# Kernel optimization log

Hardware: AMD Instinct MI355X
Metric: run time of the kernel (lower is better)

## Reference

```python
import jax, jax.numpy as jnp
import numpy as np

NUM_GRAPHS = 256
BN_EPS = 1e-5
GN_EPS = 1e-5


def setup_inputs() -> dict:
    key = jax.random.key(0)
    ks = jax.random.split(key, 8)
    N, E, D, H = 100000, 600000, 128, 128
    x = jax.random.normal(ks[0], (N, D), dtype=jnp.float32)
    W1 = jax.random.normal(ks[1], (4, 4 * H, D), dtype=jnp.float32) * 0.05
    bn_g = jnp.ones((4, 4 * H), dtype=jnp.float32)
    bn_b = jnp.zeros((4, 4 * H), dtype=jnp.float32)
    W2 = jax.random.normal(ks[2], (4, H, 4 * H), dtype=jnp.float32) * 0.05
    b2 = jnp.zeros((4, H), dtype=jnp.float32)
    gn_g = jnp.ones((4, H), dtype=jnp.float32)
    gn_b = jnp.zeros((4, H), dtype=jnp.float32)
    gn_a = jnp.ones((4, H), dtype=jnp.float32)
    edge_index = jax.random.randint(ks[3], (2, E), 0, N, dtype=jnp.int64)
    batch = jnp.sort(jax.random.randint(ks[4], (N,), 0, NUM_GRAPHS, dtype=jnp.int64))
    return {"x": x, "W1": W1, "bn_g": bn_g, "bn_b": bn_b, "W2": W2, "b2": b2,
            "gn_g": gn_g, "gn_b": gn_b, "gn_a": gn_a,
            "edge_index": edge_index, "batch": batch}


def reference(x, W1, bn_g, bn_b, W2, b2, gn_g, gn_b, gn_a, edge_index, batch):
    N = x.shape[0]
    src, dst = edge_index[0], edge_index[1]
    # per-graph node counts (shared by GraphNorm and mean-pool)
    cnt = jax.ops.segment_sum(jnp.ones((N,), x.dtype), batch, num_segments=NUM_GRAPHS)
    cnt = jnp.maximum(cnt, 1.0)[:, None]  # [G,1]

    h = x
    hs = []
    for l in range(4):  # fixed small layer loop
        # GINConv: (1+eps)*x + sum_{j->i} x_j, eps=0 default
        agg = jax.ops.segment_sum(h[src], dst, num_segments=N)
        z = h + agg
        # MLP: Linear(no bias) -> BatchNorm1d (batch stats) -> SELU -> Linear
        z = z @ W1[l].T
        mu = jnp.mean(z, axis=0)
        var = jnp.mean((z - mu) ** 2, axis=0)
        z = (z - mu) * jax.lax.rsqrt(var + BN_EPS) * bn_g[l] + bn_b[l]
        z = jax.nn.selu(z)
        z = z @ W2[l].T + b2[l]
        # GraphNorm: per-graph mean/var with learnable mean scale alpha
        gmean = jax.ops.segment_sum(z, batch, num_segments=NUM_GRAPHS) / cnt
        sub = z - gn_a[l] * gmean[batch]
        gvar = jax.ops.segment_sum(sub * sub, batch, num_segments=NUM_GRAPHS) / cnt
        z = gn_g[l] * sub * jax.lax.rsqrt(gvar[batch] + GN_EPS) + gn_b[l]
        z = jax.nn.selu(z)  # self.act (SELU, matching MLP)
        hs.append(z)
        h = z

    hg = jnp.concatenate(hs, axis=1)  # [N, 4*H]
    pooled = jax.ops.segment_sum(hg, batch, num_segments=NUM_GRAPHS) / cnt
    return pooled
```

## Files before the change

### kernel.cpp

```cpp
#include <hip/hip_runtime.h>
#include <hip/hip_bf16.h>


typedef __attribute__((ext_vector_type(8))) short bf16x8;
typedef __attribute__((ext_vector_type(4))) float f32x4;

__device__ __forceinline__ unsigned short f2b(float x){
    __hip_bfloat16 h = __float2bfloat16(x);
    return *reinterpret_cast<unsigned short*>(&h);
}
__device__ __forceinline__ float b2f(unsigned short u){
    __hip_bfloat16 h;
    *reinterpret_cast<unsigned short*>(&h) = u;
    return __bfloat162float(h);
}
__device__ __forceinline__ float selu_f(float x){
    const float sc = 1.0507009873554805f, al = 1.6732632423543772f;
    return x > 0.f ? sc * x : sc * al * (__expf(x) - 1.f);
}

__global__ void count_kernel(const int* __restrict__ dst, int* __restrict__ counts, int E){
    int e = blockIdx.x * 256 + threadIdx.x;
    if (e < E) atomicAdd(&counts[dst[e]], 1);
}

__global__ void cnt_bs_kernel(const int* __restrict__ batch, float* __restrict__ cnt, int N){
    __shared__ int sb[257];
    int g = threadIdx.x;
    int lo = 0, hi = N;
    while (lo < hi){ int mid = (lo + hi) >> 1; if (batch[mid] < g) lo = mid + 1; else hi = mid; }
    sb[g] = lo;
    if (g == 0) sb[256] = N;
    __syncthreads();
    cnt[g] = fmaxf((float)(sb[g + 1] - sb[g]), 1.f);
}

__global__ __launch_bounds__(1024) void scan_kernel(const int* __restrict__ counts,
                                                    int* __restrict__ row_ptr, int N){
    __shared__ int wsum[16];
    __shared__ int wpre[16];
    __shared__ int s_total;
    __shared__ int s_running;
    int tid = threadIdx.x;
    int lane = tid & 63, wid = tid >> 6;
    if (tid == 0) s_running = 0;
    __syncthreads();
    for (int base = 0; base < N; base += 4096){
        int idx0 = base + tid * 4;
        int v[4];
        #pragma unroll
        for (int j = 0; j < 4; j++) v[j] = (idx0 + j < N) ? counts[idx0 + j] : 0;
        int tsum = v[0] + v[1] + v[2] + v[3];
        int x = tsum;
        #pragma unroll
        for (int off = 1; off < 64; off <<= 1){
            int y = __shfl_up(x, off, 64);
            if (lane >= off) x += y;
        }
        if (lane == 63) wsum[wid] = x;
        __syncthreads();
        if (wid == 0 && lane < 16){
            int w = wsum[lane];
            int xx = w;
            #pragma unroll
            for (int off = 1; off < 16; off <<= 1){
                int y = __shfl_up(xx, off, 64);
                if (lane >= off) xx += y;
            }
            wpre[lane] = xx - w;
            if (lane == 15) s_total = xx;
        }
        __syncthreads();
        int run = s_running + wpre[wid] + (x - tsum);
        #pragma unroll
        for (int j = 0; j < 4; j++){
            if (idx0 + j < N) row_ptr[idx0 + j] = run;
            run += v[j];
        }
        __syncthreads();
        if (tid == 0) s_running += s_total;
        __syncthreads();
    }
    if (tid == 0) row_ptr[N] = s_running;
}

__global__ void fill_kernel(const int* __restrict__ ei, const int* __restrict__ row_ptr,
                            int* __restrict__ fill, int* __restrict__ colv, int E){
    int e = blockIdx.x * 256 + threadIdx.x;
    if (e < E){
        int s = ei[e];
        int d = ei[E + e];
        int pos = atomicAdd(&fill[d], 1);
        colv[row_ptr[d] + pos] = s;
    }
}

__global__ void pack_kernel(const float* __restrict__ W1, const float* __restrict__ W2,
                            unsigned short* __restrict__ W1p, unsigned short* __restrict__ W2p){
    int t = blockIdx.x * 256 + threadIdx.x;
    int which = t >> 15;
    int u = t & 32767;
    int lane = u & 63; u >>= 6;
    int nf = u & 3; u >>= 2;
    int wc = u & 1; u >>= 1;
    int kk = u & 3; u >>= 2;
    int c = u & 3; u >>= 2;
    int l = u;
    int col = wc * 64 + nf * 16 + (lane & 15);
    int kbase = kk * 32 + (lane >> 4) * 8;
    size_t ob = ((((((size_t)(l * 4 + c) * 4 + kk) * 2 + wc) * 4 + nf) * 2) * 512) + lane * 8;
    unsigned short* dst = which == 0 ? W1p : W2p;
    #pragma unroll
    for (int j = 0; j < 8; j++){
        int k = kbase + j;
        float wv = which == 0 ? W1[((size_t)(l * 512) + c * 128 + col) * 128 + k]
                              : W2[((size_t)(l * 128) + col) * 512 + c * 128 + k];
        unsigned short hi = f2b(wv);
        unsigned short lo = f2b(wv - b2f(hi));
        dst[ob + j] = hi;
        dst[ob + 512 + j] = lo;
    }
}

__global__ __launch_bounds__(256) void agg_split_kernel(
    const float* __restrict__ h, const int* __restrict__ row_ptr,
    const int* __restrict__ colv,
    unsigned short* __restrict__ zhi, unsigned short* __restrict__ zlo, int N)
{
    int t = blockIdx.x * 256 + threadIdx.x;
    int i = t >> 5;
    if (i >= N) return;
    int vo = (t & 31);
    const float4* hv = reinterpret_cast<const float4*>(h);
    int p0 = row_ptr[i], p1 = row_ptr[i + 1];
    float4 acc = hv[(size_t)i * 32 + vo];
    int p = p0;
    for (; p + 4 <= p1; p += 4){
        int s0 = colv[p], s1 = colv[p + 1], s2 = colv[p + 2], s3 = colv[p + 3];
        float4 a = hv[(size_t)s0 * 32 + vo];
        float4 b = hv[(size_t)s1 * 32 + vo];
        float4 c = hv[(size_t)s2 * 32 + vo];
        float4 d = hv[(size_t)s3 * 32 + vo];
        acc.x += (a.x + b.x) + (c.x + d.x);
        acc.y += (a.y + b.y) + (c.y + d.y);
        acc.z += (a.z + b.z) + (c.z + d.z);
        acc.w += (a.w + b.w) + (c.w + d.w);
    }
    for (; p < p1; p++){
        float4 a = hv[(size_t)colv[p] * 32 + vo];
        acc.x += a.x; acc.y += a.y; acc.z += a.z; acc.w += a.w;
    }
    float vals[4] = {acc.x, acc.y, acc.z, acc.w};
    unsigned int h01, h23, l01, l23;
    {
        unsigned short hh[4], ll[4];
        #pragma unroll
        for (int j = 0; j < 4; j++){
            hh[j] = f2b(vals[j]);
            ll[j] = f2b(vals[j] - b2f(hh[j]));
        }
        h01 = (unsigned int)hh[0] | ((unsigned int)hh[1] << 16);
        h23 = (unsigned int)hh[2] | ((unsigned int)hh[3] << 16);
        l01 = (unsigned int)ll[0] | ((unsigned int)ll[1] << 16);
        l23 = (unsigned int)ll[2] | ((unsigned int)ll[3] << 16);
    }
    int kk = vo >> 3, kg = (vo >> 1) & 3, half = vo & 1;
    size_t fo = ((size_t)(i >> 4) * 4 + kk) * 512 + (kg * 16 + (i & 15)) * 8 + half * 4;
    *reinterpret_cast<uint2*>(zhi + fo) = make_uint2(h01, h23);
    *reinterpret_cast<uint2*>(zlo + fo) = make_uint2(l01, l23);
}

__global__ __launch_bounds__(512) void stats_k(
    const unsigned short* __restrict__ Zhi_g, const unsigned short* __restrict__ Zlo_g,
    const unsigned short* __restrict__ Bp, float* __restrict__ bn_acc, int N)
{
    __shared__ __align__(16) unsigned short Zh_s[16384];
    __shared__ __align__(16) unsigned short Zl_s[16384];
    int tid = threadIdx.x, lane = tid & 63, w = tid >> 6;
    int wr = w >> 2, wq = w & 3;
    int r_lo = lane & 15, kg = lane >> 4;
    int m0 = blockIdx.x * 128;

    {
        size_t gbase = (size_t)(m0 >> 4) * 2048;
        const uint4* gh = reinterpret_cast<const uint4*>(Zhi_g + gbase);
        const uint4* gl = reinterpret_cast<const uint4*>(Zlo_g + gbase);
        uint4* sh4 = reinterpret_cast<uint4*>(Zh_s);
        uint4* sl4 = reinterpret_cast<uint4*>(Zl_s);
        #pragma unroll
        for (int j = 0; j < 4; j++){
            sh4[j * 512 + tid] = gh[j * 512 + tid];
            sl4[j * 512 + tid] = gl[j * 512 + tid];
        }
    }
    __syncthreads();

    int wc = wq >> 1;
    for (int c = 0; c < 4; c++){
        const bf16x8* Bv = reinterpret_cast<const bf16x8*>(Bp) + (size_t)c * 4096;
        f32x4 acc[4][2];
        #pragma unroll
        for (int i = 0; i < 4; i++)
            #pragma unroll
            for (int j = 0; j < 2; j++) acc[i][j] = (f32x4){0.f, 0.f, 0.f, 0.f};

        for (int kk = 0; kk < 4; kk++){
            bf16x8 bh[2], bl[2];
            #pragma unroll
            for (int nf = 0; nf < 2; nf++){
                int nfold = (wq & 1) * 2 + nf;
                int ob = ((kk * 2 + wc) * 4 + nfold) * 2;
                bh[nf] = Bv[(ob + 0) * 64 + lane];
                bl[nf] = Bv[(ob + 1) * 64 + lane];
            }
            bf16x8 ah[4], alr[4];
            #pragma unroll
            for (int mf = 0; mf < 4; mf++){
                int so = ((wr * 4 + mf) * 4 + kk) * 512 + lane * 8;
                ah[mf]  = *reinterpret_cast<const bf16x8*>(&Zh_s[so]);
                alr[mf] = *reinterpret_cast<const bf16x8*>(&Zl_s[so]);
            }
            #pragma unroll
            for (int mf = 0; mf < 4; mf++)
                #pragma unroll
                for (int nf = 0; nf < 2; nf++){
                    acc[mf][nf] = __builtin_amdgcn_mfma_f32_16x16x32_bf16(ah[mf],  bh[nf], acc[mf][nf], 0, 0, 0);
                    acc[mf][nf] = __builtin_amdgcn_mfma_f32_16x16x32_bf16(ah[mf],  bl[nf], acc[mf][nf], 0, 0, 0);
                    acc[mf][nf] = __builtin_amdgcn_mfma_f32_16x16x32_bf16(alr[mf], bh[nf], acc[mf][nf], 0, 0, 0);
                }
        }

        #pragma unroll
        for (int nf = 0; nf < 2; nf++){
            int col = wq * 32 + nf * 16 + r_lo;
            float s = 0.f, q = 0.f;
            #pragma unroll
            for (int mf = 0; mf < 4; mf++)
                #pragma unroll
                for (int r = 0; r < 4; r++){
                    int row = m0 + wr * 64 + mf * 16 + kg * 4 + r;
                    if (row < N){
                        float v = acc[mf][nf][r];
                        s += v; q += v * v;
                    }
                }
            s += __shfl_xor(s, 16); s += __shfl_xor(s, 32);
            q += __shfl_xor(q, 16); q += __shfl_xor(q, 32);
            if (lane < 16){
                atomicAdd(&bn_acc[c * 256 + col], s);
                atomicAdd(&bn_acc[c * 256 + 128 + col], q);
            }
        }
    }
}

__global__ void bn_final_k(const float* __restrict__ bn_acc,
                           const float* __restrict__ bng, const float* __restrict__ bnb,
                           float* __restrict__ sc, float* __restrict__ sh,
                           int l, float invN){
    int colg = threadIdx.x;
    float s = bn_acc[(colg >> 7) * 256 + (colg & 127)];
    float q = bn_acc[(colg >> 7) * 256 + 128 + (colg & 127)];
    float mu = s * invN;
    float var = q * invN - mu * mu;
    float inv = rsqrtf(var + 1e-5f);
    float g = bng[l * 512 + colg] * inv;
    sc[colg] = g;
    sh[colg] = bnb[l * 512 + colg] - mu * g;
}

__global__ __launch_bounds__(512, 1) void fused_k(
    const unsigned short* __restrict__ Zhi_g, const unsigned short* __restrict__ Zlo_g,
    const unsigned short* __restrict__ B1p, const unsigned short* __restrict__ B2p,
    float* __restrict__ Z, const float* __restrict__ bsc, const float* __restrict__ bsh,
    const float* __restrict__ b2l, int N)
{
    __shared__ __align__(16) unsigned short Zh_s[16384];
    __shared__ __align__(16) unsigned short Zl_s[16384];
    __shared__ __align__(16) unsigned short Ph[128][136];
    __shared__ __align__(16) unsigned short Pl[128][136];
    __shared__ float s_sc[512], s_sh[512];
    int tid = threadIdx.x, lane = tid & 63, w = tid >> 6;
    int wr = w >> 2, wq = w & 3;
    int r_lo = lane & 15, kg = lane >> 4;
    int m0 = blockIdx.x * 128;

    if (tid < 512){ s_sc[tid] = bsc[tid]; s_sh[tid] = bsh[tid]; }
    {
        size_t gbase = (size_t)(m0 >> 4) * 2048;
        const uint4* gh = reinterpret_cast<const uint4*>(Zhi_g + gbase);
        const uint4* gl = reinterpret_cast<const uint4*>(Zlo_g + gbase);
        uint4* sh4 = reinterpret_cast<uint4*>(Zh_s);
        uint4* sl4 = reinterpret_cast<uint4*>(Zl_s);
        #pragma unroll
        for (int j = 0; j < 4; j++){
            sh4[j * 512 + tid] = gh[j * 512 + tid];
            sl4[j * 512 + tid] = gl[j * 512 + tid];
        }
    }
    __syncthreads();

    int wc = wq >> 1;
    f32x4 acc2[4][2];
    #pragma unroll
    for (int i = 0; i < 4; i++)
        #pragma unroll
        for (int j = 0; j < 2; j++) acc2[i][j] = (f32x4){0.f, 0.f, 0.f, 0.f};

    for (int c = 0; c < 4; c++){
        f32x4 acc1[2][4];
        #pragma unroll
        for (int i = 0; i < 2; i++)
            #pragma unroll
            for (int j = 0; j < 4; j++) acc1[i][j] = (f32x4){0.f, 0.f, 0.f, 0.f};

        const bf16x8* B1v = reinterpret_cast<const bf16x8*>(B1p) + (size_t)c * 4096;
        for (int kk = 0; kk < 4; kk++){
            bf16x8 awh[2], awl[2];
            #pragma unroll
            for (int mfp = 0; mfp < 2; mfp++){
                int colblk = wq * 2 + mfp;
                int wc1 = colblk >> 2, nf1 = colblk & 3;
                int ob = ((kk * 2 + wc1) * 4 + nf1) * 2;
                awh[mfp] = B1v[(ob + 0) * 64 + lane];
                awl[mfp] = B1v[(ob + 1) * 64 + lane];
            }
            bf16x8 bzh[4], bzl[4];
            #pragma unroll
            for (int nfp = 0; nfp < 4; nfp++){
                int so = ((wr * 4 + nfp) * 4 + kk) * 512 + lane * 8;
                bzh[nfp] = *reinterpret_cast<const bf16x8*>(&Zh_s[so]);
                bzl[nfp] = *reinterpret_cast<const bf16x8*>(&Zl_s[so]);
            }
            #pragma unroll
            for (int mfp = 0; mfp < 2; mfp++)
                #pragma unroll
                for (int nfp = 0; nfp < 4; nfp++){
                    acc1[mfp][nfp] = __builtin_amdgcn_mfma_f32_16x16x32_bf16(awh[mfp], bzh[nfp], acc1[mfp][nfp], 0, 0, 0);
                    acc1[mfp][nfp] = __builtin_amdgcn_mfma_f32_16x16x32_bf16(awh[mfp], bzl[nfp], acc1[mfp][nfp], 0, 0, 0);
                    acc1[mfp][nfp] = __builtin_amdgcn_mfma_f32_16x16x32_bf16(awl[mfp], bzh[nfp], acc1[mfp][nfp], 0, 0, 0);
                }
        }

        __syncthreads();
        #pragma unroll
        for (int mfp = 0; mfp < 2; mfp++){
            int ckb = wq * 32 + mfp * 16 + kg * 4;
            float sc0 = s_sc[c * 128 + ckb + 0], sh0 = s_sh[c * 128 + ckb + 0];
            float sc1 = s_sc[c * 128 + ckb + 1], sh1 = s_sh[c * 128 + ckb + 1];
            float sc2 = s_sc[c * 128 + ckb + 2], sh2 = s_sh[c * 128 + ckb + 2];
            float sc3 = s_sc[c * 128 + ckb + 3], sh3 = s_sh[c * 128 + ckb + 3];
            #pragma unroll
            for (int nfp = 0; nfp < 4; nfp++){
                float t0 = selu_f(fmaf(acc1[mfp][nfp][0], sc0, sh0));
                float t1 = selu_f(fmaf(acc1[mfp][nfp][1], sc1, sh1));
                float t2 = selu_f(fmaf(acc1[mfp][nfp][2], sc2, sh2));
                float t3 = selu_f(fmaf(acc1[mfp][nfp][3], sc3, sh3));
                unsigned short h0 = f2b(t0), h1 = f2b(t1), h2 = f2b(t2), h3 = f2b(t3);
                unsigned short l0 = f2b(t0 - b2f(h0)), l1 = f2b(t1 - b2f(h1));
                unsigned short l2 = f2b(t2 - b2f(h2)), l3 = f2b(t3 - b2f(h3));
                int node = wr * 64 + nfp * 16 + r_lo;
                uint2 hv = make_uint2((unsigned int)h0 | ((unsigned int)h1 << 16),
                                      (unsigned int)h2 | ((unsigned int)h3 << 16));
                uint2 lv = make_uint2((unsigned int)l0 | ((unsigned int)l1 << 16),
                                      (unsigned int)l2 | ((unsigned int)l3 << 16));
                *reinterpret_cast<uint2*>(&Ph[node][ckb]) = hv;
                *reinterpret_cast<uint2*>(&Pl[node][ckb]) = lv;
            }
        }
        __syncthreads();

        const bf16x8* B2v = reinterpret_cast<const bf16x8*>(B2p);
        for (int kk2 = 0; kk2 < 4; kk2++){
            int kkf = c * 4 + kk2;
            bf16x8 bh[2], bl[2];
            #pragma unroll
            for (int nf = 0; nf < 2; nf++){
                int nfold = (wq & 1) * 2 + nf;
                int ob = ((kkf * 2 + wc) * 4 + nfold) * 2;
                bh[nf] = B2v[(ob + 0) * 64 + lane];
                bl[nf] = B2v[(ob + 1) * 64 + lane];
            }
            bf16x8 ah[4], alr[4];
            #pragma unroll
            for (int mf = 0; mf < 4; mf++){
                int ar = wr * 64 + mf * 16 + r_lo;
                ah[mf]  = *reinterpret_cast<const bf16x8*>(&Ph[ar][kk2 * 32 + kg * 8]);
                alr[mf] = *reinterpret_cast<const bf16x8*>(&Pl[ar][kk2 * 32 + kg * 8]);
            }
            #pragma unroll
            for (int mf = 0; mf < 4; mf++)
                #pragma unroll
                for (int nf = 0; nf < 2; nf++){
                    acc2[mf][nf] = __builtin_amdgcn_mfma_f32_16x16x32_bf16(ah[mf],  bh[nf], acc2[mf][nf], 0, 0, 0);
                    acc2[mf][nf] = __builtin_amdgcn_mfma_f32_16x16x32_bf16(ah[mf],  bl[nf], acc2[mf][nf], 0, 0, 0);
                    acc2[mf][nf] = __builtin_amdgcn_mfma_f32_16x16x32_bf16(alr[mf], bh[nf], acc2[mf][nf], 0, 0, 0);
                }
        }
    }

    #pragma unroll
    for (int nf = 0; nf < 2; nf++){
        int col = wq * 32 + nf * 16 + r_lo;
        float bv = b2l[col];
        #pragma unroll
        for (int mf = 0; mf < 4; mf++)
            #pragma unroll
            for (int r = 0; r < 4; r++){
                int row = m0 + wr * 64 + mf * 16 + kg * 4 + r;
                if (row < N)
                    Z[(size_t)row * 128 + col] = bv + acc2[mf][nf][r];
            }
    }
}

__global__ __launch_bounds__(256) void gn_stats_kernel(
    const float* __restrict__ z2, const int* __restrict__ batch,
    float* __restrict__ gsum, float* __restrict__ gsq, int N)
{
    __shared__ int sb[128];
    int tid = threadIdx.x;
    int base = blockIdx.x * 128;
    int end = min(128, N - base);
    if (tid < 128) sb[tid] = (tid < end) ? batch[base + tid] : 0;
    __syncthreads();
    int vo = tid & 31;
    int r0 = (tid >> 5) * 16;
    if (r0 >= end) return;
    int rend = min(r0 + 16, end);
    const float4* zv = reinterpret_cast<const float4*>(z2);
    float sx = 0.f, sy = 0.f, sz = 0.f, sw = 0.f;
    float qx = 0.f, qy = 0.f, qz = 0.f, qw = 0.f;
    int run_g = sb[r0];
    for (int r = r0; r < rend; r++){
        int g = sb[r];
        if (g != run_g){
            float* gs = &gsum[run_g * 128 + vo * 4];
            float* gq = &gsq[run_g * 128 + vo * 4];
            atomicAdd(gs + 0, sx); atomicAdd(gs + 1, sy); atomicAdd(gs + 2, sz); atomicAdd(gs + 3, sw);
            atomicAdd(gq + 0, qx); atomicAdd(gq + 1, qy); atomicAdd(gq + 2, qz); atomicAdd(gq + 3, qw);
            sx = sy = sz = sw = 0.f; qx = qy = qz = qw = 0.f;
            run_g = g;
        }
        float4 v = zv[(size_t)(base + r) * 32 + vo];
        sx += v.x; sy += v.y; sz += v.z; sw += v.w;
        qx += v.x * v.x; qy += v.y * v.y; qz += v.z * v.z; qw += v.w * v.w;
    }
    float* gs = &gsum[run_g * 128 + vo * 4];
    float* gq = &gsq[run_g * 128 + vo * 4];
    atomicAdd(gs + 0, sx); atomicAdd(gs + 1, sy); atomicAdd(gs + 2, sz); atomicAdd(gs + 3, sw);
    atomicAdd(gq + 0, qx); atomicAdd(gq + 1, qy); atomicAdd(gq + 2, qz); atomicAdd(gq + 3, qw);
}

__global__ void gn_final_kernel(float* __restrict__ gsum, float* __restrict__ gsq,
                                const float* __restrict__ cnt,
                                const float* __restrict__ gng, const float* __restrict__ gnb,
                                const float* __restrict__ gna,
                                float* __restrict__ scale, float* __restrict__ shift, int l){
    int g = blockIdx.x, c = threadIdx.x;
    int idx = g * 128 + c;
    float n = cnt[g];
    float m = gsum[idx] / n;
    float e2 = gsq[idx] / n;
    float a = gna[l * 128 + c];
    float var = e2 - (2.f * a - a * a) * m * m;
    float inv = rsqrtf(var + 1e-5f);
    float sc = gng[l * 128 + c] * inv;
    scale[idx] = sc;
    shift[idx] = gnb[l * 128 + c] - a * m * sc;
    gsum[idx] = 0.f;
    gsq[idx] = 0.f;
}

__global__ __launch_bounds__(256) void gn_apply_kernel(
    float* __restrict__ z2h, const int* __restrict__ batch,
    const float* __restrict__ scale, const float* __restrict__ shift,
    float* __restrict__ pool, int l, int N)
{
    __shared__ int sb[128];
    int tid = threadIdx.x;
    int base = blockIdx.x * 128;
    int end = min(128, N - base);
    if (tid < 128) sb[tid] = (tid < end) ? batch[base + tid] : 0;
    __syncthreads();
    int vo = tid & 31;
    int r0 = (tid >> 5) * 16;
    if (r0 >= end) return;
    int rend = min(r0 + 16, end);
    float4* zv = reinterpret_cast<float4*>(z2h);
    int run_g = sb[r0];
    float scx = scale[run_g * 128 + vo * 4 + 0], shx = shift[run_g * 128 + vo * 4 + 0];
    float scy = scale[run_g * 128 + vo * 4 + 1], shy = shift[run_g * 128 + vo * 4 + 1];
    float scz = scale[run_g * 128 + vo * 4 + 2], shz = shift[run_g * 128 + vo * 4 + 2];
    float scw = scale[run_g * 128 + vo * 4 + 3], shw = shift[run_g * 128 + vo * 4 + 3];
    float px = 0.f, py = 0.f, pz = 0.f, pw = 0.f;
    for (int r = r0; r < rend; r++){
        int g = sb[r];
        if (g != run_g){
            float* pp = &pool[run_g * 512 + l * 128 + vo * 4];
            atomicAdd(pp + 0, px); atomicAdd(pp + 1, py); atomicAdd(pp + 2, pz); atomicAdd(pp + 3, pw);
            px = py = pz = pw = 0.f;
            run_g = g;
            scx = scale[g * 128 + vo * 4 + 0]; shx = shift[g * 128 + vo * 4 + 0];
            scy = scale[g * 128 + vo * 4 + 1]; shy = shift[g * 128 + vo * 4 + 1];
            scz = scale[g * 128 + vo * 4 + 2]; shz = shift[g * 128 + vo * 4 + 2];
            scw = scale[g * 128 + vo * 4 + 3]; shw = shift[g * 128 + vo * 4 + 3];
        }
        size_t idx = (size_t)(base + r) * 32 + vo;
        float4 v = zv[idx];
        v.x = selu_f(fmaf(v.x, scx, shx));
        v.y = selu_f(fmaf(v.y, scy, shy));
        v.z = selu_f(fmaf(v.z, scz, shz));
        v.w = selu_f(fmaf(v.w, scw, shw));
        zv[idx] = v;
        px += v.x; py += v.y; pz += v.z; pw += v.w;
    }
    float* pp = &pool[run_g * 512 + l * 128 + vo * 4];
    atomicAdd(pp + 0, px); atomicAdd(pp + 1, py); atomicAdd(pp + 2, pz); atomicAdd(pp + 3, pw);
}

__global__ void final_kernel(const float* __restrict__ pool, const float* __restrict__ cnt,
                             float* __restrict__ out, int n){
    int i = blockIdx.x * 256 + threadIdx.x;
    if (i < n) out[i] = pool[i] / cnt[i >> 9];
}

extern "C" void kernel_launch(void* const* d_in, const int* in_sizes, int n_in,
                              void* d_out, int out_size, void* d_ws, size_t ws_size,
                              hipStream_t stream){
    const float* x    = (const float*)d_in[0];
    const float* W1   = (const float*)d_in[1];
    const float* bng  = (const float*)d_in[2];
    const float* bnb  = (const float*)d_in[3];
    const float* W2   = (const float*)d_in[4];
    const float* b2   = (const float*)d_in[5];
    const float* gng  = (const float*)d_in[6];
    const float* gnb  = (const float*)d_in[7];
    const float* gna  = (const float*)d_in[8];
    const int*   ei   = (const int*)d_in[9];
    const int*   batch= (const int*)d_in[10];
    int N = in_sizes[0] / 128;
    int E = in_sizes[9] / 2;
    float* out = (float*)d_out;
    int RB = (N + 127) / 128;

    char* ws = (char*)d_ws;
    size_t off = 0;
    auto alloc = [&](size_t bytes) -> char* {
        char* p = ws + off;
        off += (bytes + 255) & ~(size_t)255;
        return p;
    };
    unsigned short* z0hi = (unsigned short*)alloc((size_t)RB * 128 * 128 * 2);
    unsigned short* z0lo = (unsigned short*)alloc((size_t)RB * 128 * 128 * 2);
    float* z2     = (float*)alloc((size_t)N * 128 * 4);
    unsigned short* W1p = (unsigned short*)alloc(524288 * 2);
    unsigned short* W2p = (unsigned short*)alloc(524288 * 2);
    int*   row_ptr= (int*)alloc((size_t)(N + 1) * 4);
    int*   colv   = (int*)alloc((size_t)E * 4);
    int*   counts = (int*)alloc((size_t)N * 4);
    int*   fill   = (int*)alloc((size_t)N * 4);
    float* cnt_f  = (float*)alloc(256 * 4);
    float* bn_acc = (float*)alloc(16 * 256 * 4);
    float* bn_sc  = (float*)alloc(512 * 4);
    float* bn_sh  = (float*)alloc(512 * 4);
    float* gn_sum = (float*)alloc(256 * 128 * 4);
    float* gn_sq  = (float*)alloc(256 * 128 * 4);
    float* gn_sc  = (float*)alloc(256 * 128 * 4);
    float* gn_sh  = (float*)alloc(256 * 128 * 4);
    float* pool   = (float*)alloc(256 * 512 * 4);
    (void)ws_size;

    hipMemsetAsync(counts, 0, (size_t)N * 4, stream);
    hipMemsetAsync(fill,   0, (size_t)N * 4, stream);
    hipMemsetAsync(bn_acc, 0, 16 * 256 * 4, stream);
    hipMemsetAsync(gn_sum, 0, 2 * 256 * 128 * 4, stream);
    hipMemsetAsync(pool,   0, 256 * 512 * 4, stream);
    {
        size_t tail_start = (size_t)(N >> 4) * 2048;
        size_t total      = (size_t)RB * 128 * 128;
        if (total > tail_start){
            size_t tail_bytes = (total - tail_start) * 2;
            hipMemsetAsync(z0hi + tail_start, 0, tail_bytes, stream);
            hipMemsetAsync(z0lo + tail_start, 0, tail_bytes, stream);
        }
    }

    pack_kernel<<<256, 256, 0, stream>>>(W1, W2, W1p, W2p);
    count_kernel<<<(E + 255) / 256, 256, 0, stream>>>(ei + E, counts, E);
    scan_kernel<<<1, 1024, 0, stream>>>(counts, row_ptr, N);
    fill_kernel<<<(E + 255) / 256, 256, 0, stream>>>(ei, row_ptr, fill, colv, E);
    cnt_bs_kernel<<<1, 256, 0, stream>>>(batch, cnt_f, N);

    const float* hcur = x;
    float invN = 1.f / (float)N;
    for (int l = 0; l < 4; l++){
        agg_split_kernel<<<(N + 7) / 8, 256, 0, stream>>>(hcur, row_ptr, colv, z0hi, z0lo, N);
        stats_k<<<RB, 512, 0, stream>>>(z0hi, z0lo, W1p + (size_t)l * 131072,
                                        bn_acc + l * 1024, N);
        bn_final_k<<<1, 512, 0, stream>>>(bn_acc + l * 1024, bng, bnb,
                                          bn_sc, bn_sh, l, invN);
        fused_k<<<RB, 512, 0, stream>>>(z0hi, z0lo, W1p + (size_t)l * 131072,
                                        W2p + (size_t)l * 131072, z2,
                                        bn_sc, bn_sh, b2 + l * 128, N);
        gn_stats_kernel<<<RB, 256, 0, stream>>>(z2, batch, gn_sum, gn_sq, N);
        gn_final_kernel<<<256, 128, 0, stream>>>(gn_sum, gn_sq, cnt_f, gng, gnb, gna,
                                                 gn_sc, gn_sh, l);
        gn_apply_kernel<<<RB, 256, 0, stream>>>(z2, batch, gn_sc, gn_sh, pool, l, N);
        hcur = z2;
    }
    final_kernel<<<(out_size + 255) / 256, 256, 0, stream>>>(pool, cnt_f, out, out_size);
}
```

Measured before the change: 1.475 ms.

## Compute BatchNorm stats from input second moments instead of full first GEMM

Replaces the stats pass, which recomputed the full N×512 first-layer GEMM to get BatchNorm mean and variance, with a Gram-matrix pass. It accumulates Z^T Z (128×128) and column sums of the aggregated input with a persistent grid. Per-channel mean and variance are then derived as w·colsum/N and wᵀMw/N, which cuts the MFMA work of the stats pass by roughly four times. The cost is a partial-sum buffer plus an extra reduce kernel, transposed shared-memory reads that may hit bank conflicts, and variance computed as E[z²]−μ², which can lose precision.

```diff
diff --git a/kernel.cpp b/kernel.cpp
--- a/kernel.cpp
+++ b/kernel.cpp
@@ -4,6 +4,8 @@
 
 typedef __attribute__((ext_vector_type(8))) short bf16x8;
 typedef __attribute__((ext_vector_type(4))) float f32x4;
+
+#define MOMB 256
 
 __device__ __forceinline__ unsigned short f2b(float x){
     __hip_bfloat16 h = __float2bfloat16(x);
@@ -170,103 +172,148 @@
     *reinterpret_cast<uint2*>(zlo + fo) = make_uint2(l01, l23);
 }
 
-__global__ __launch_bounds__(512) void stats_k(
+__device__ __forceinline__ bf16x8 tread(const unsigned short* __restrict__ s, int base){
+    union { bf16x8 v; unsigned short u[8]; } r;
+    #pragma unroll
+    for (int j = 0; j < 8; j++) r.u[j] = s[base + j * 8];
+    return r.v;
+}
+
+__global__ __launch_bounds__(256) void moment_k(
     const unsigned short* __restrict__ Zhi_g, const unsigned short* __restrict__ Zlo_g,
-    const unsigned short* __restrict__ Bp, float* __restrict__ bn_acc, int N)
+    float* __restrict__ Mpart, float* __restrict__ cpart, int RB)
 {
     __shared__ __align__(16) unsigned short Zh_s[16384];
     __shared__ __align__(16) unsigned short Zl_s[16384];
+    __shared__ float cs[256];
     int tid = threadIdx.x, lane = tid & 63, w = tid >> 6;
-    int wr = w >> 2, wq = w & 3;
-    int r_lo = lane & 15, kg = lane >> 4;
-    int m0 = blockIdx.x * 128;
-
-    {
-        size_t gbase = (size_t)(m0 >> 4) * 2048;
-        const uint4* gh = reinterpret_cast<const uint4*>(Zhi_g + gbase);
-        const uint4* gl = reinterpret_cast<const uint4*>(Zlo_g + gbase);
-        uint4* sh4 = reinterpret_cast<uint4*>(Zh_s);
-        uint4* sl4 = reinterpret_cast<uint4*>(Zl_s);
-        #pragma unroll
-        for (int j = 0; j < 4; j++){
-            sh4[j * 512 + tid] = gh[j * 512 + tid];
-            sl4[j * 512 + tid] = gl[j * 512 + tid];
-        }
-    }
-    __syncthreads();
-
-    int wc = wq >> 1;
-    for (int c = 0; c < 4; c++){
-        const bf16x8* Bv = reinterpret_cast<const bf16x8*>(Bp) + (size_t)c * 4096;
-        f32x4 acc[4][2];
-        #pragma unroll
-        for (int i = 0; i < 4; i++)
-            #pragma unroll
-            for (int j = 0; j < 2; j++) acc[i][j] = (f32x4){0.f, 0.f, 0.f, 0.f};
-
-        for (int kk = 0; kk < 4; kk++){
-            bf16x8 bh[2], bl[2];
-            #pragma unroll
-            for (int nf = 0; nf < 2; nf++){
-                int nfold = (wq & 1) * 2 + nf;
-                int ob = ((kk * 2 + wc) * 4 + nfold) * 2;
-                bh[nf] = Bv[(ob + 0) * 64 + lane];
-                bl[nf] = Bv[(ob + 1) * 64 + lane];
-            }
-            bf16x8 ah[4], alr[4];
-            #pragma unroll
-            for (int mf = 0; mf < 4; mf++){
-                int so = ((wr * 4 + mf) * 4 + kk) * 512 + lane * 8;
-                ah[mf]  = *reinterpret_cast<const bf16x8*>(&Zh_s[so]);
-                alr[mf] = *reinterpret_cast<const bf16x8*>(&Zl_s[so]);
-            }
-            #pragma unroll
-            for (int mf = 0; mf < 4; mf++)
+    int fl = lane & 15, g = lane >> 4;
+    int tpart = (g >> 1) * 2048 + (g & 1) * 64;
+    int fpart = (fl >> 3) * 128 + (fl & 7);
+
+    f32x4 acc[2][8];
+    #pragma unroll
+    for (int i = 0; i < 2; i++)
+        #pragma unroll
+        for (int j = 0; j < 8; j++) acc[i][j] = (f32x4){0.f, 0.f, 0.f, 0.f};
+    float csum = 0.f;
+    int cf = tid & 127, chalf = tid >> 7;
+    int cfbase = (cf >> 5) * 512 + ((cf >> 3) & 3) * 128 + (cf & 7);
+
+    for (int blk = blockIdx.x; blk < RB; blk += MOMB){
+        __syncthreads();
+        {
+            size_t gbase = (size_t)blk * 16384;
+            const uint4* gh = reinterpret_cast<const uint4*>(Zhi_g + gbase);
+            const uint4* gl = reinterpret_cast<const uint4*>(Zlo_g + gbase);
+            uint4* sh4 = reinterpret_cast<uint4*>(Zh_s);
+            uint4* sl4 = reinterpret_cast<uint4*>(Zl_s);
+            #pragma unroll
+            for (int j = 0; j < 8; j++){
+                sh4[j * 256 + tid] = gh[j * 256 + tid];
+                sl4[j * 256 + tid] = gl[j * 256 + tid];
+            }
+        }
+        __syncthreads();
+
+        #pragma unroll 8
+        for (int n = chalf * 64; n < chalf * 64 + 64; n++){
+            int addr = (n >> 4) * 2048 + (n & 15) * 8 + cfbase;
+            csum += b2f(Zh_s[addr]) + b2f(Zl_s[addr]);
+        }
+
+        for (int nk = 0; nk < 4; nk++){
+            int nb = nk * 4096 + tpart + fpart;
+            bf16x8 ath[2], atl[2];
+            #pragma unroll
+            for (int i = 0; i < 2; i++){
+                int ft = w * 2 + i;
+                int base = nb + (ft >> 1) * 512 + (ft & 1) * 256;
+                ath[i] = tread(Zh_s, base);
+                atl[i] = tread(Zl_s, base);
+            }
+            #pragma unroll
+            for (int ft2 = 0; ft2 < 8; ft2++){
+                int base2 = nb + (ft2 >> 1) * 512 + (ft2 & 1) * 256;
+                bf16x8 bth = tread(Zh_s, base2);
+                bf16x8 btl = tread(Zl_s, base2);
                 #pragma unroll
-                for (int nf = 0; nf < 2; nf++){
-                    acc[mf][nf] = __builtin_amdgcn_mfma_f32_16x16x32_bf16(ah[mf],  bh[nf], acc[mf][nf], 0, 0, 0);
-                    acc[mf][nf] = __builtin_amdgcn_mfma_f32_16x16x32_bf16(ah[mf],  bl[nf], acc[mf][nf], 0, 0, 0);
-                    acc[mf][nf] = __builtin_amdgcn_mfma_f32_16x16x32_bf16(alr[mf], bh[nf], acc[mf][nf], 0, 0, 0);
+                for (int i = 0; i < 2; i++){
+                    acc[i][ft2] = __builtin_amdgcn_mfma_f32_16x16x32_bf16(ath[i], bth, acc[i][ft2], 0, 0, 0);
+                    acc[i][ft2] = __builtin_amdgcn_mfma_f32_16x16x32_bf16(ath[i], btl, acc[i][ft2], 0, 0, 0);
+                    acc[i][ft2] = __builtin_amdgcn_mfma_f32_16x16x32_bf16(atl[i], bth, acc[i][ft2], 0, 0, 0);
                 }
-        }
-
-        #pragma unroll
-        for (int nf = 0; nf < 2; nf++){
-            int col = wq * 32 + nf * 16 + r_lo;
-            float s = 0.f, q = 0.f;
-            #pragma unroll
-            for (int mf = 0; mf < 4; mf++)
-                #pragma unroll
-                for (int r = 0; r < 4; r++){
-                    int row = m0 + wr * 64 + mf * 16 + kg * 4 + r;
-                    if (row < N){
-                        float v = acc[mf][nf][r];
-                        s += v; q += v * v;
-                    }
-                }
-            s += __shfl_xor(s, 16); s += __shfl_xor(s, 32);
-            q += __shfl_xor(q, 16); q += __shfl_xor(q, 32);
-            if (lane < 16){
-                atomicAdd(&bn_acc[c * 256 + col], s);
-                atomicAdd(&bn_acc[c * 256 + 128 + col], q);
-            }
-        }
-    }
-}
-
-__global__ void bn_final_k(const float* __restrict__ bn_acc,
-                           const float* __restrict__ bng, const float* __restrict__ bnb,
-                           float* __restrict__ sc, float* __restrict__ sh,
-                           int l, float invN){
-    int colg = threadIdx.x;
-    float s = bn_acc[(colg >> 7) * 256 + (colg & 127)];
-    float q = bn_acc[(colg >> 7) * 256 + 128 + (colg & 127)];
-    float mu = s * invN;
-    float var = q * invN - mu * mu;
-    float inv = rsqrtf(var + 1e-5f);
-    float g = bng[l * 512 + colg] * inv;
-    sc[colg] = g;
-    sh[colg] = bnb[l * 512 + colg] - mu * g;
+            }
+        }
+    }
+
+    float* Mp = Mpart + (size_t)blockIdx.x * 16384;
+    int col = lane & 15, rbase = (lane >> 4) * 4;
+    #pragma unroll
+    for (int i = 0; i < 2; i++)
+        #pragma unroll
+        for (int ft2 = 0; ft2 < 8; ft2++)
+            #pragma unroll
+            for (int r = 0; r < 4; r++){
+                int a = (w * 2 + i) * 16 + rbase + r;
+                int b = ft2 * 16 + col;
+                Mp[a * 128 + b] = acc[i][ft2][r];
+            }
+    cs[tid] = csum;
+    __syncthreads();
+    if (tid < 128) cpart[(size_t)blockIdx.x * 128 + tid] = cs[tid] + cs[tid + 128];
+}
+
+__global__ __launch_bounds__(256) void reduce_k(
+    const float* __restrict__ Mpart, const float* __restrict__ cpart,
+    float* __restrict__ Msum, float* __restrict__ colsum)
+{
+    int gid = blockIdx.x * 256 + threadIdx.x;
+    float s = 0.f;
+    for (int p = 0; p < MOMB; p++) s += Mpart[(size_t)p * 16384 + gid];
+    Msum[gid] = s;
+    if (blockIdx.x == 0 && threadIdx.x < 128){
+        float c = 0.f;
+        for (int p = 0; p < MOMB; p++) c += cpart[(size_t)p * 128 + threadIdx.x];
+        colsum[threadIdx.x] = c;
+    }
+}
+
+__global__ __launch_bounds__(128) void bn_final2_k(
+    const float* __restrict__ Msum, const float* __restrict__ colsum,
+    const float* __restrict__ W1, const float* __restrict__ bng,
+    const float* __restrict__ bnb, float* __restrict__ sc, float* __restrict__ sh,
+    int l, float invN)
+{
+    __shared__ float s_w[128];
+    __shared__ float red[4];
+    int j = blockIdx.x;
+    int t = threadIdx.x;
+    float wt = W1[(size_t)l * 65536 + (size_t)j * 128 + t];
+    s_w[t] = wt;
+    __syncthreads();
+    float y = 0.f;
+    #pragma unroll 4
+    for (int k = 0; k < 128; k++) y = fmaf(Msum[t * 128 + k], s_w[k], y);
+    float p = wt * y;
+    float mc = wt * colsum[t];
+    #pragma unroll
+    for (int off = 32; off >= 1; off >>= 1){
+        p += __shfl_xor(p, off, 64);
+        mc += __shfl_xor(mc, off, 64);
+    }
+    int lane = t & 63, wv = t >> 6;
+    if (lane == 0){ red[wv * 2] = p; red[wv * 2 + 1] = mc; }
+    __syncthreads();
+    if (t == 0){
+        float e2 = (red[0] + red[2]) * invN;
+        float mu = (red[1] + red[3]) * invN;
+        float var = e2 - mu * mu;
+        float inv = rsqrtf(var + 1e-5f);
+        float gg = bng[l * 512 + j] * inv;
+        sc[j] = gg;
+        sh[j] = bnb[l * 512 + j] - mu * gg;
+    }
 }
 
 __global__ __launch_bounds__(512, 1) void fused_k(
@@ -561,7 +608,10 @@
     int*   counts = (int*)alloc((size_t)N * 4);
     int*   fill   = (int*)alloc((size_t)N * 4);
     float* cnt_f  = (float*)alloc(256 * 4);
-    float* bn_acc = (float*)alloc(16 * 256 * 4);
+    float* Mpart  = (float*)alloc((size_t)MOMB * 16384 * 4);
+    float* cpart  = (float*)alloc((size_t)MOMB * 128 * 4);
+    float* Msum   = (float*)alloc(16384 * 4);
+    float* colsum = (float*)alloc(128 * 4);
     float* bn_sc  = (float*)alloc(512 * 4);
     float* bn_sh  = (float*)alloc(512 * 4);
     float* gn_sum = (float*)alloc(256 * 128 * 4);
@@ -573,7 +623,6 @@
 
     hipMemsetAsync(counts, 0, (size_t)N * 4, stream);
     hipMemsetAsync(fill,   0, (size_t)N * 4, stream);
-    hipMemsetAsync(bn_acc, 0, 16 * 256 * 4, stream);
     hipMemsetAsync(gn_sum, 0, 2 * 256 * 128 * 4, stream);
     hipMemsetAsync(pool,   0, 256 * 512 * 4, stream);
     {
@@ -596,10 +645,10 @@
     float invN = 1.f / (float)N;
     for (int l = 0; l < 4; l++){
         agg_split_kernel<<<(N + 7) / 8, 256, 0, stream>>>(hcur, row_ptr, colv, z0hi, z0lo, N);
-        stats_k<<<RB, 512, 0, stream>>>(z0hi, z0lo, W1p + (size_t)l * 131072,
-                                        bn_acc + l * 1024, N);
-        bn_final_k<<<1, 512, 0, stream>>>(bn_acc + l * 1024, bng, bnb,
-                                          bn_sc, bn_sh, l, invN);
+        moment_k<<<MOMB, 256, 0, stream>>>(z0hi, z0lo, Mpart, cpart, RB);
+        reduce_k<<<64, 256, 0, stream>>>(Mpart, cpart, Msum, colsum);
+        bn_final2_k<<<512, 128, 0, stream>>>(Msum, colsum, W1, bng, bnb,
+                                             bn_sc, bn_sh, l, invN);
         fused_k<<<RB, 512, 0, stream>>>(z0hi, z0lo, W1p + (size_t)l * 131072,
                                         W2p + (size_t)l * 131072, z2,
                                         bn_sc, bn_sh, b2 + l * 128, N);
```

Result: no change. 1.475 ms (-0.0%).
